# Performance work log

Measured on AMD Instinct MI355X. Metric: run time of the kernel, lower is better.

## Reference

```python
import jax, jax.numpy as jnp
import numpy as np

IN_F = 256
OUT_F = 64
ALPHA = 0.2  # LeakyReLU negative slope
MASK_VAL = -9e15


def _glorot(key, shape):
    r = np.sqrt(6.0 / (shape[0] + shape[1]))
    return jax.random.uniform(key, shape, jnp.float32, -r, r)


def setup_inputs() -> dict:
    key = jax.random.key(0)
    k_h, k_adj, k_W, k_a = jax.random.split(key, 4)
    B, N = 4, 4096
    h = jax.random.normal(k_h, (B, N, IN_F), jnp.float32)
    adj = jax.random.randint(k_adj, (B, N, N), 0, 2, jnp.int32)
    W = _glorot(k_W, (IN_F, OUT_F))
    a = _glorot(k_a, (2 * OUT_F, 1))
    bias = jnp.zeros((OUT_F,), jnp.float32)
    return {"h": h, "adj": adj, "W": W, "a": a, "bias": bias}


def reference(h, adj, W, a, bias):
    # Wh: [B, N, F_out]
    Wh = jnp.matmul(h, W) + bias
    # additive attention: e_ij = leakyrelu(Wh_i . a1 + Wh_j . a2)
    Wh1 = jnp.matmul(Wh, a[:OUT_F, :])   # [B, N, 1]
    Wh2 = jnp.matmul(Wh, a[OUT_F:, :])   # [B, N, 1]
    e = Wh1 + jnp.swapaxes(Wh2, 2, 1)    # [B, N, N]
    e = jnp.where(e > 0, e, ALPHA * e)   # LeakyReLU
    e = jnp.where(adj > 0, e, MASK_VAL)
    attention = jax.nn.softmax(e, axis=2)
    h_prime = jnp.matmul(attention, Wh)  # [B, N, F_out]
    return jax.nn.elu(h_prime)           # concat=True -> ELU
```

## Files before the change

kernel.cpp:

```cpp
#include <hip/hip_runtime.h>
#include <hip/hip_bf16.h>
#include <cstdint>

#define IN_F 256
#define OUT_F 64
#define NB 4
#define NN 4096
#define ALPHA 0.2f
#define LOG2E 1.4426950408889634f

typedef __attribute__((ext_vector_type(4))) float f32x4;
typedef __attribute__((ext_vector_type(4))) int i32x4;
typedef __attribute__((ext_vector_type(8))) short bf16x8;

static __device__ __forceinline__ ushort f2bf(float x) {
  uint32_t u = __float_as_uint(x);
  uint32_t r = (u + 0x7fffu + ((u >> 16) & 1u)) >> 16;
  return (ushort)r;
}

static __device__ __forceinline__ void gl16(const void* g, void* l) {
  __builtin_amdgcn_global_load_lds(
      (const __attribute__((address_space(1))) void*)g,
      (__attribute__((address_space(3))) void*)l, 16, 0, 0);
}

__global__ __launch_bounds__(256) void k1_gemm(
    const float* __restrict__ h, const float* __restrict__ W,
    const float* __restrict__ a, const float* __restrict__ bias,
    ushort* __restrict__ WhT, float* __restrict__ Wh1, float* __restrict__ Wh2)
{
  __shared__ float hs[32][33];
  __shared__ float Ws[32][64];
  const int t  = threadIdx.x;
  const int tx = t & 15;
  const int ty = t >> 4;
  const int row0 = blockIdx.x * 32;

  float acc[2][4] = {};

  for (int k0 = 0; k0 < IN_F; k0 += 32) {
    {
      int r = t >> 3, c4 = t & 7;
      *(f32x4*)&hs[r][c4 * 4] =
          *(const f32x4*)(h + (size_t)(row0 + r) * IN_F + k0 + c4 * 4);
    }
    #pragma unroll
    for (int s = 0; s < 2; ++s) {
      int f4 = t + 256 * s;
      int kk = f4 >> 4, c4 = f4 & 15;
      *(f32x4*)&Ws[kk][c4 * 4] = *(const f32x4*)(W + (size_t)(k0 + kk) * OUT_F + c4 * 4);
    }
    __syncthreads();
    #pragma unroll 8
    for (int kk = 0; kk < 32; ++kk) {
      f32x4 bv = *(const f32x4*)&Ws[kk][tx * 4];
      float av0 = hs[ty * 2 + 0][kk];
      float av1 = hs[ty * 2 + 1][kk];
      #pragma unroll
      for (int j = 0; j < 4; ++j) {
        acc[0][j] += av0 * bv[j];
        acc[1][j] += av1 * bv[j];
      }
    }
    __syncthreads();
  }

  #pragma unroll
  for (int i = 0; i < 2; ++i) {
    int row = row0 + ty * 2 + i;
    float s1 = 0.f, s2 = 0.f;
    #pragma unroll
    for (int j = 0; j < 4; ++j) {
      float v = acc[i][j] + bias[tx * 4 + j];
      acc[i][j] = v;
      s1 += v * a[tx * 4 + j];
      s2 += v * a[64 + tx * 4 + j];
    }
    #pragma unroll
    for (int off = 1; off < 16; off <<= 1) {
      s1 += __shfl_xor(s1, off);
      s2 += __shfl_xor(s2, off);
    }
    if (tx == 0) { Wh1[row] = s1 * LOG2E; Wh2[row] = s2 * LOG2E; }
    int bb = row >> 12;
    int n  = row & 4095;
    #pragma unroll
    for (int j = 0; j < 4; ++j) {
      WhT[(((size_t)(bb * OUT_F + tx * 4 + j)) << 12) + n] = f2bf(acc[i][j]);
    }
  }
}

#define BUFSZ 24576
#define NDEPTH 5
#define WH2_OFF 122880
#define LDS_TOTAL 139264
__global__ __launch_bounds__(512) void k2_attn(
    const int* __restrict__ adj, const ushort* __restrict__ WhT,
    const float* __restrict__ Wh1, const float* __restrict__ Wh2,
    float* __restrict__ out)
{
  extern __shared__ char smem[];
  const int t  = threadIdx.x;
  const int l  = t & 63;
  const int w  = t >> 6;
  const int rq = w >> 1;
  const int kq = w & 1;
  const int g  = l >> 4;
  const int lr = l & 15;
  const int b  = blockIdx.y;
  const int r0 = blockIdx.x << 6;

  const int   rowl  = rq * 16 + lr;
  const float wh1 = Wh1[(b << 12) + r0 + rowl];
  asm volatile("" :: "v"(wh1));

  const int*    adjb = adj + ((size_t)b << 24) + ((size_t)r0 << 12);
  const ushort* whb  = WhT + ((size_t)(b * OUT_F) << 12);
  const int rowA = t >> 4,           mlA = (t & 15) ^ (rowA & 7);
  const int rowB = (t + 512) >> 4,   mlB = (t & 15) ^ (rowB & 7);
  const int fW   = t >> 3,           mlW = (t & 7) ^ (fW & 7);
  const int*    srcA = adjb + (size_t)rowA * 4096 + mlA * 4;
  const int*    srcB = adjb + (size_t)rowB * 4096 + mlB * 4;
  const ushort* srcW = whb + ((size_t)fW << 12) + mlW * 8;
  const int ldsA = t << 4, ldsB = (t + 512) << 4, ldsW = 16384 + (t << 4);

  auto STAGE = [&](int s) {
    char* base = smem + (s % NDEPTH) * BUFSZ;
    gl16(srcA + s * 64, base + ldsA);
    gl16(srcB + s * 64, base + ldsB);
    gl16(srcW + s * 64, base + ldsW);
  };

  f32x4 a0 = {0.f,0.f,0.f,0.f}, a1 = {0.f,0.f,0.f,0.f};
  f32x4 a2 = {0.f,0.f,0.f,0.f}, a3 = {0.f,0.f,0.f,0.f};
  f32x4 as = {0.f,0.f,0.f,0.f};
  bf16x8 ones;
  #pragma unroll
  for (int i = 0; i < 8; ++i) ones[i] = (short)0x3F80;

  const int swzA = (rowl & 7) << 4;
  const int swzW = (lr & 7) << 4;
  const int offA0 = (kq * 128 + g * 32) ^ swzA;
  const int offA1 = (kq * 128 + g * 32 + 16) ^ swzA;
  const int offW  = (kq * 64 + g * 16) ^ swzW;

  auto COMPUTE = [&](int s) {
    const char* base = smem + (s % NDEPTH) * BUFSZ;
    i32x4 ad0 = *(const i32x4*)(base + rowl * 256 + offA0);
    i32x4 ad1 = *(const i32x4*)(base + rowl * 256 + offA1);
    const char* wb = base + 16384;
    bf16x8 b0 = *(const bf16x8*)(wb + (lr     ) * 128 + offW);
    bf16x8 b1 = *(const bf16x8*)(wb + (lr + 16) * 128 + offW);
    bf16x8 b2 = *(const bf16x8*)(wb + (lr + 32) * 128 + offW);
    bf16x8 b3 = *(const bf16x8*)(wb + (lr + 48) * 128 + offW);
    const char* w2b = smem + WH2_OFF + (s << 8) + kq * 128 + g * 32;
    f32x4 w20 = *(const f32x4*)(w2b);
    f32x4 w21 = *(const f32x4*)(w2b + 16);

    float p[8];
    #pragma unroll
    for (int i = 0; i < 8; ++i) {
      float w2 = (i < 4) ? w20[i] : w21[i - 4];
      int   am = (i < 4) ? ad0[i] : ad1[i - 4];
      float s_ = wh1 + w2;
      float lk = fmaf(ALPHA, fminf(s_, 0.f), fmaxf(s_, 0.f));
      float pe = exp2f(lk);
      p[i] = (am > 0) ? pe : 0.0f;
    }
    union { bf16x8 v; uint32_t u[4]; } af;
    #pragma unroll
    for (int i = 0; i < 4; ++i)
      asm("v_cvt_pk_bf16_f32 %0, %1, %2" : "=v"(af.u[i]) : "v"(p[2*i]), "v"(p[2*i+1]));

    as = __builtin_amdgcn_mfma_f32_16x16x32_bf16(af.v, ones, as, 0, 0, 0);
    a0 = __builtin_amdgcn_mfma_f32_16x16x32_bf16(af.v, b0,   a0, 0, 0, 0);
    a1 = __builtin_amdgcn_mfma_f32_16x16x32_bf16(af.v, b1,   a1, 0, 0, 0);
    a2 = __builtin_amdgcn_mfma_f32_16x16x32_bf16(af.v, b2,   a2, 0, 0, 0);
    a3 = __builtin_amdgcn_mfma_f32_16x16x32_bf16(af.v, b3,   a3, 0, 0, 0);
  };

  {
    const float* w2src = Wh2 + (b << 12);
    gl16(w2src + (t << 2),         smem + WH2_OFF + (t << 4));
    gl16(w2src + ((t + 512) << 2), smem + WH2_OFF + ((t + 512) << 4));
  }
  STAGE(0);
  STAGE(1);
  STAGE(2);
  STAGE(3);

  for (int s = 0; s < 64; ++s) {
    if (s < 61)      asm volatile("s_waitcnt vmcnt(9)" ::: "memory");
    else if (s == 61) asm volatile("s_waitcnt vmcnt(6)" ::: "memory");
    else if (s == 62) asm volatile("s_waitcnt vmcnt(3)" ::: "memory");
    else              asm volatile("s_waitcnt vmcnt(0)" ::: "memory");
    __builtin_amdgcn_s_barrier();
    COMPUTE(s);
    if (s < 60) STAGE(s + 4);
  }

  __syncthreads();
  float* sacc = (float*)smem;
  float* ssum = (float*)(smem + 34816);
  #pragma unroll
  for (int r = 0; r < 4; ++r) {
    int rr = rq * 16 + g * 4 + r;
    float* dst = sacc + (kq * 64 + rr) * 68;
    dst[ 0 + lr] = a0[r];
    dst[16 + lr] = a1[r];
    dst[32 + lr] = a2[r];
    dst[48 + lr] = a3[r];
    if (lr == 0) ssum[kq * 64 + rr] = as[r];
  }
  __syncthreads();

  const int row = t >> 3;
  const int c0  = (t & 7) << 3;
  const float* p0 = sacc + row * 68;
  const float* p1 = sacc + (64 + row) * 68;
  float d = ssum[row] + ssum[64 + row];
  float inv = 1.0f / d;
  f32x4 o0, o1;
  #pragma unroll
  for (int j = 0; j < 4; ++j) {
    float x = (p0[c0 + j] + p1[c0 + j]) * inv;
    o0[j] = x > 0.f ? x : expm1f(x);
    float y = (p0[c0 + 4 + j] + p1[c0 + 4 + j]) * inv;
    o1[j] = y > 0.f ? y : expm1f(y);
  }
  size_t ob = ((size_t)((b << 12) + r0 + row) << 6) + c0;
  *(f32x4*)(out + ob)     = o0;
  *(f32x4*)(out + ob + 4) = o1;
}

extern "C" void kernel_launch(void* const* d_in, const int* in_sizes, int n_in,
                              void* d_out, int out_size, void* d_ws, size_t ws_size,
                              hipStream_t stream) {
  const float* h    = (const float*)d_in[0];
  const int*   adj  = (const int*)d_in[1];
  const float* W    = (const float*)d_in[2];
  const float* a    = (const float*)d_in[3];
  const float* bias = (const float*)d_in[4];
  float* out = (float*)d_out;

  char* ws = (char*)d_ws;
  ushort* WhT = (ushort*)ws;
  float*  Wh1 = (float*)(ws + (size_t)NB * OUT_F * NN * 2);
  float*  Wh2 = Wh1 + NB * NN;

  (void)hipFuncSetAttribute((const void*)k2_attn,
                            hipFuncAttributeMaxDynamicSharedMemorySize, LDS_TOTAL);

  k1_gemm<<<dim3(NB * NN / 32), 256, 0, stream>>>(h, W, a, bias, WhT, Wh1, Wh2);
  k2_attn<<<dim3(NN / 64, NB), 512, LDS_TOTAL, stream>>>(adj, WhT, Wh1, Wh2, out);
}
```

Baseline: 75.35 us.

## Split attention reduction over key dimension into two partitions with separate reduce kernel

The attention kernel now splits the 4096-column key range into two halves via a third grid dimension. Each block writes unnormalized partial accumulators and row sums to workspace, and a new reduce kernel combines them and applies normalization and ELU. The pipeline depth drops from 5 to 3 stages and LDS shrinks, so more blocks can be resident per CU (launch bounds now request 4). The aim is to double the grid and fill the GPU's CUs better, at the cost of an extra launch, extra global traffic for the partials, and shallower prefetch.

New measurement: 76.13 us. About the same (+1.0%).

```diff
diff --git a/kernel.cpp b/kernel.cpp
--- a/kernel.cpp
+++ b/kernel.cpp
@@ -93,13 +93,13 @@
 }
 
 #define BUFSZ 24576
-#define NDEPTH 5
-#define WH2_OFF 122880
-#define LDS_TOTAL 139264
-__global__ __launch_bounds__(512) void k2_attn(
+#define NDEPTH 3
+#define WH2_OFF 73728
+#define LDS_TOTAL 81920
+__global__ __launch_bounds__(512, 4) void k2_attn(
     const int* __restrict__ adj, const ushort* __restrict__ WhT,
     const float* __restrict__ Wh1, const float* __restrict__ Wh2,
-    float* __restrict__ out)
+    float* __restrict__ pacc, float* __restrict__ psum)
 {
   extern __shared__ char smem[];
   const int t  = threadIdx.x;
@@ -111,13 +111,14 @@
   const int lr = l & 15;
   const int b  = blockIdx.y;
   const int r0 = blockIdx.x << 6;
-
-  const int   rowl  = rq * 16 + lr;
-  const float wh1 = Wh1[(b << 12) + r0 + rowl];
+  const int z  = blockIdx.z;
+
+  const int   rowl = rq * 16 + lr;
+  const float wh1  = Wh1[(b << 12) + r0 + rowl];
   asm volatile("" :: "v"(wh1));
 
-  const int*    adjb = adj + ((size_t)b << 24) + ((size_t)r0 << 12);
-  const ushort* whb  = WhT + ((size_t)(b * OUT_F) << 12);
+  const int*    adjb = adj + ((size_t)b << 24) + ((size_t)r0 << 12) + (z << 11);
+  const ushort* whb  = WhT + ((size_t)(b * OUT_F) << 12) + (z << 11);
   const int rowA = t >> 4,           mlA = (t & 15) ^ (rowA & 7);
   const int rowB = (t + 512) >> 4,   mlB = (t & 15) ^ (rowB & 7);
   const int fW   = t >> 3,           mlW = (t & 7) ^ (fW & 7);
@@ -182,23 +183,18 @@
   };
 
   {
-    const float* w2src = Wh2 + (b << 12);
-    gl16(w2src + (t << 2),         smem + WH2_OFF + (t << 4));
-    gl16(w2src + ((t + 512) << 2), smem + WH2_OFF + ((t + 512) << 4));
+    const float* w2src = Wh2 + (b << 12) + (z << 11);
+    gl16(w2src + (t << 2), smem + WH2_OFF + (t << 4));
   }
   STAGE(0);
   STAGE(1);
-  STAGE(2);
-  STAGE(3);
-
-  for (int s = 0; s < 64; ++s) {
-    if (s < 61)      asm volatile("s_waitcnt vmcnt(9)" ::: "memory");
-    else if (s == 61) asm volatile("s_waitcnt vmcnt(6)" ::: "memory");
-    else if (s == 62) asm volatile("s_waitcnt vmcnt(3)" ::: "memory");
-    else              asm volatile("s_waitcnt vmcnt(0)" ::: "memory");
+
+  for (int s = 0; s < 32; ++s) {
+    if (s < 31) asm volatile("s_waitcnt vmcnt(3)" ::: "memory");
+    else        asm volatile("s_waitcnt vmcnt(0)" ::: "memory");
     __builtin_amdgcn_s_barrier();
     COMPUTE(s);
-    if (s < 60) STAGE(s + 4);
+    if (s < 30) STAGE(s + 2);
   }
 
   __syncthreads();
@@ -221,18 +217,34 @@
   const float* p0 = sacc + row * 68;
   const float* p1 = sacc + (64 + row) * 68;
   float d = ssum[row] + ssum[64 + row];
-  float inv = 1.0f / d;
   f32x4 o0, o1;
   #pragma unroll
   for (int j = 0; j < 4; ++j) {
-    float x = (p0[c0 + j] + p1[c0 + j]) * inv;
-    o0[j] = x > 0.f ? x : expm1f(x);
-    float y = (p0[c0 + 4 + j] + p1[c0 + 4 + j]) * inv;
-    o1[j] = y > 0.f ? y : expm1f(y);
-  }
-  size_t ob = ((size_t)((b << 12) + r0 + row) << 6) + c0;
-  *(f32x4*)(out + ob)     = o0;
-  *(f32x4*)(out + ob + 4) = o1;
+    o0[j] = p0[c0 + j] + p1[c0 + j];
+    o1[j] = p0[c0 + 4 + j] + p1[c0 + 4 + j];
+  }
+  size_t pb = ((size_t)z << 20) + (((size_t)(b << 12) + r0 + row) << 6) + c0;
+  *(f32x4*)(pacc + pb)     = o0;
+  *(f32x4*)(pacc + pb + 4) = o1;
+  if ((t & 7) == 0) psum[(z << 14) + (b << 12) + r0 + row] = d;
+}
+
+__global__ __launch_bounds__(256) void k3_reduce(
+    const float* __restrict__ pacc, const float* __restrict__ psum,
+    float* __restrict__ out)
+{
+  const int e4  = (blockIdx.x * 256 + threadIdx.x) << 2;
+  const int row = e4 >> 6;
+  f32x4 v0 = *(const f32x4*)(pacc + e4);
+  f32x4 v1 = *(const f32x4*)(pacc + (1 << 20) + e4);
+  float inv = 1.0f / (psum[row] + psum[16384 + row]);
+  f32x4 o;
+  #pragma unroll
+  for (int j = 0; j < 4; ++j) {
+    float x = (v0[j] + v1[j]) * inv;
+    o[j] = x > 0.f ? x : expm1f(x);
+  }
+  *(f32x4*)(out + e4) = o;
 }
 
 extern "C" void kernel_launch(void* const* d_in, const int* in_sizes, int n_in,
@@ -249,10 +261,13 @@
   ushort* WhT = (ushort*)ws;
   float*  Wh1 = (float*)(ws + (size_t)NB * OUT_F * NN * 2);
   float*  Wh2 = Wh1 + NB * NN;
+  float*  pacc = Wh2 + NB * NN;
+  float*  psum = pacc + (2 << 20);
 
   (void)hipFuncSetAttribute((const void*)k2_attn,
                             hipFuncAttributeMaxDynamicSharedMemorySize, LDS_TOTAL);
 
   k1_gemm<<<dim3(NB * NN / 32), 256, 0, stream>>>(h, W, a, bias, WhT, Wh1, Wh2);
-  k2_attn<<<dim3(NN / 64, NB), 512, LDS_TOTAL, stream>>>(adj, WhT, Wh1, Wh2, out);
-}
+  k2_attn<<<dim3(NN / 64, NB, 2), 512, LDS_TOTAL, stream>>>(adj, WhT, Wh1, Wh2, pacc, psum);
+  k3_reduce<<<dim3(1024), 256, 0, stream>>>(pacc, psum, out);
+}
```
